# Kernel optimization log

Measured on AMD Instinct MI355X. Metric: run time of the kernel, lower is better.

Reference implementation:

```python
import jax, jax.numpy as jnp
import numpy as np
import math

B, L, D_MODEL = 8, 1024, 512
D_INNER = 1024          # expand*d_model
D2 = D_INNER // 2       # per-branch channels
DT_RANK = 32            # ceil(d_model/16)
D_STATE = 16
K = 4                   # d_conv
HIDDEN = 4 * D_MODEL


def setup_inputs() -> dict:
    key = jax.random.key(0)
    ks = jax.random.split(key, 12)
    rn = lambda k, s, sc: jax.random.normal(k, s, jnp.float32) * sc
    x = rn(ks[0], (B, L, D_MODEL), 1.0)
    in_proj_w = rn(ks[1], (D_INNER, D_MODEL), D_MODEL ** -0.5)
    conv_x_w = rn(ks[2], (D2, 1, K), 0.2)
    conv_z_w = rn(ks[3], (D2, 1, K), 0.2)
    x_proj_w = rn(ks[4], (DT_RANK + 2 * D_STATE, D2), D2 ** -0.5)
    dt_proj_w = rn(ks[5], (D2, DT_RANK), DT_RANK ** -0.5)
    dt = jnp.exp(jax.random.uniform(ks[6], (D2,)) * (math.log(0.1) - math.log(0.001)) + math.log(0.001))
    dt_proj_b = dt + jnp.log(-jnp.expm1(-dt))  # inverse softplus
    A_log = jnp.log(jnp.tile(jnp.arange(1, D_STATE + 1, dtype=jnp.float32)[None, :], (D2, 1)))
    ssm_D = jnp.ones((D2,), jnp.float32)
    out_proj_w = rn(ks[7], (D_MODEL, D_INNER), D_INNER ** -0.5)
    fc1_w = rn(ks[8], (HIDDEN, D_MODEL), D_MODEL ** -0.5)
    fc2_w = rn(ks[9], (D_MODEL, HIDDEN), HIDDEN ** -0.5)
    return dict(x=x,
                ln1_w=jnp.ones((D_MODEL,)), ln1_b=jnp.zeros((D_MODEL,)),
                in_proj_w=in_proj_w, conv_x_w=conv_x_w, conv_z_w=conv_z_w,
                x_proj_w=x_proj_w, dt_proj_w=dt_proj_w, dt_proj_b=dt_proj_b,
                A_log=A_log, ssm_D=ssm_D, out_proj_w=out_proj_w,
                ln2_w=jnp.ones((D_MODEL,)), ln2_b=jnp.zeros((D_MODEL,)),
                fc1_w=fc1_w, fc1_b=jnp.zeros((HIDDEN,)),
                fc2_w=fc2_w, fc2_b=jnp.zeros((D_MODEL,)))


def _layernorm(x, w, b, eps=1e-5):
    m = jnp.mean(x, -1, keepdims=True)
    v = jnp.mean((x - m) ** 2, -1, keepdims=True)
    return (x - m) * jax.lax.rsqrt(v + eps) * w + b


def _dwconv1d_same(x, w):
    # x: (b, c, l); w: (c, 1, K). torch 'same' for even K pads (left=1, right=2)
    return jax.lax.conv_general_dilated(
        x, w, window_strides=(1,), padding=[(1, 2)],
        dimension_numbers=('NCH', 'OIH', 'NCH'), feature_group_count=x.shape[1])


def _selective_scan(u, delta, A, Bc, Cc, Dp):
    # u, delta: (b, d, l); A: (d, n); Bc, Cc: (b, n, l); Dp: (d,)
    dA = jnp.exp(delta[..., None] * A[None, :, None, :])            # (b,d,l,n)
    Bt = jnp.moveaxis(Bc, 2, 1)                                     # (b,l,n)
    dBu = (delta * u)[..., None] * Bt[:, None, :, :]                # (b,d,l,n)
    dA_l = jnp.moveaxis(dA, 2, 0)                                   # (l,b,d,n)
    dBu_l = jnp.moveaxis(dBu, 2, 0)

    def step(h, t):
        dAt, dBut = t
        h = dAt * h + dBut
        return h, h

    h0 = jnp.zeros((u.shape[0], u.shape[1], A.shape[1]), u.dtype)
    _, hs = jax.lax.scan(step, h0, (dA_l, dBu_l))                   # hs: (l,b,d,n)
    Ct = jnp.moveaxis(Cc, 2, 0)                                     # (l,b,n)
    y = jnp.einsum('lbdn,lbn->bdl', hs, Ct)
    return y + Dp[None, :, None] * u


def _mixer(xn, in_proj_w, conv_x_w, conv_z_w, x_proj_w, dt_proj_w, dt_proj_b, A_log, ssm_D, out_proj_w):
    # xn: (b, l, d_model)
    xz = jnp.einsum('bld,ed->bel', xn, in_proj_w)                   # (b, d_inner, l)
    xh, zh = jnp.split(xz, 2, axis=1)                               # (b, d2, l) each
    xh = jax.nn.silu(_dwconv1d_same(xh, conv_x_w))
    zh = jax.nn.silu(_dwconv1d_same(zh, conv_z_w))
    x_dbl = jnp.einsum('bdl,rd->brl', xh, x_proj_w)                 # (b, R+2n, l)
    dt, Bc, Cc = jnp.split(x_dbl, [DT_RANK, DT_RANK + D_STATE], axis=1)
    dt = jnp.einsum('brl,dr->bdl', dt, dt_proj_w)
    delta = jax.nn.softplus(dt + dt_proj_b[None, :, None])          # delta_bias + delta_softplus
    A = -jnp.exp(A_log)
    y = _selective_scan(xh, delta, A, Bc, Cc, ssm_D)                # (b, d2, l)
    out = jnp.concatenate([y, zh], axis=1)                          # (b, d_inner, l)
    return jnp.einsum('bdl,ed->ble', out, out_proj_w)               # (b, l, d_model)


def reference(x, ln1_w, ln1_b, in_proj_w, conv_x_w, conv_z_w, x_proj_w, dt_proj_w, dt_proj_b,
              A_log, ssm_D, out_proj_w, ln2_w, ln2_b, fc1_w, fc1_b, fc2_w, fc2_b):
    h = x + _mixer(_layernorm(x, ln1_w, ln1_b), in_proj_w, conv_x_w, conv_z_w,
                   x_proj_w, dt_proj_w, dt_proj_b, A_log, ssm_D, out_proj_w)
    h2 = _layernorm(h, ln2_w, ln2_b)
    mlp = jax.nn.gelu(h2 @ fc1_w.T + fc1_b, approximate=False) @ fc2_w.T + fc2_b
    return h + mlp
```

## Files before the change

kernel.cpp:

```cpp
#include <hip/hip_runtime.h>
#include <stdint.h>


#define MROWS 8192
#define LSEQ 1024
#define DMODEL 512
#define DINNER 1024
#define D2 512
#define NSTATE 16
#define HIDDEN 2048
#define NCHUNK 32
#define LCHUNK 32

typedef unsigned short us;
typedef short short8 __attribute__((ext_vector_type(8)));
typedef float floatx4 __attribute__((ext_vector_type(4)));

__device__ __forceinline__ us f2bf(float f) {
    unsigned int u = __float_as_uint(f);
    u = (u + 0x7fffu + ((u >> 16) & 1u)) >> 16;
    return (us)u;
}
__device__ __forceinline__ float bf2f(us u) {
    return __uint_as_float(((unsigned int)u) << 16);
}

__device__ __forceinline__ void g2lds16(const void* g, void* l) {
    typedef __attribute__((address_space(1))) void GV;
    typedef __attribute__((address_space(3))) void LV;
    GV* gp = (GV*)(uintptr_t)g;
    LV* lp = (LV*)(uint32_t)(uintptr_t)l;
    __builtin_amdgcn_global_load_lds(gp, lp, 16, 0, 0);
}

__device__ __forceinline__ void pack_slot(const float* __restrict__ w,
                                          us* __restrict__ dst, int K, int sig)
{
    int lane = sig & 63;
    int KS = K >> 5;
    int ks = (sig >> 6) % KS;
    int g = sig / (KS << 6);
    const float* src = w + (size_t)(g * 16 + (lane & 15)) * K
                         + ks * 32 + (lane >> 4) * 8;
    short8 o;
    #pragma unroll
    for (int e = 0; e < 8; e++) o[e] = (short)f2bf(src[e]);
    *(short8*)(dst + (size_t)sig * 8) = o;
}

__global__ __launch_bounds__(256) void cvt_pack6(
    const float* __restrict__ w0, const float* __restrict__ w1,
    const float* __restrict__ w2, const float* __restrict__ w3,
    const float* __restrict__ w4, const float* __restrict__ w5,
    us* __restrict__ o0, us* __restrict__ o1, us* __restrict__ o2,
    us* __restrict__ o3, us* __restrict__ o4, us* __restrict__ o5)
{
    int bx = blockIdx.x, t = threadIdx.x;
    if (bx < 256)        pack_slot(w0, o0, 512,  bx * 256 + t);
    else if (bx < 272)   pack_slot(w1, o1, 512,  (bx - 256) * 256 + t);
    else if (bx < 280)   pack_slot(w2, o2, 32,   (bx - 272) * 256 + t);
    else if (bx < 536)   pack_slot(w3, o3, 1024, (bx - 280) * 256 + t);
    else if (bx < 1048)  pack_slot(w4, o4, 512,  (bx - 536) * 256 + t);
    else                 pack_slot(w5, o5, 2048, (bx - 1048) * 256 + t);
}

__global__ __launch_bounds__(256) void ln_pack(
    const float* __restrict__ x, const float* __restrict__ w,
    const float* __restrict__ b, us* __restrict__ outp)
{
    int g = blockIdx.x, t = threadIdx.x;
    __shared__ float T[16][516];
    __shared__ float mu[16], rs[16];
    const float* src = x + (size_t)g * 16 * DMODEL;
    #pragma unroll
    for (int p = 0; p < 8; p++) {
        int idx4 = p * 256 + t;
        int row = idx4 >> 7, c = (idx4 & 127) << 2;
        float4 v = *(const float4*)(src + (size_t)row * DMODEL + c);
        *(float4*)&T[row][c] = v;
    }
    __syncthreads();
    int r = t >> 4, i = t & 15;
    float s = 0.f, ss = 0.f;
    #pragma unroll
    for (int c = 0; c < 32; c++) {
        float v = T[r][c * 16 + i];
        s += v; ss += v * v;
    }
    #pragma unroll
    for (int off = 8; off > 0; off >>= 1) {
        s += __shfl_down(s, off, 16);
        ss += __shfl_down(ss, off, 16);
    }
    if (i == 0) {
        float m = s * (1.f / DMODEL);
        mu[r] = m;
        rs[r] = rsqrtf(ss * (1.f / DMODEL) - m * m + 1e-5f);
    }
    __syncthreads();
    #pragma unroll
    for (int s0 = 0; s0 < 4; s0++) {
        int sig = t * 4 + s0;
        int lane = sig & 63, ks = sig >> 6;
        int lr = lane & 15, lq = lane >> 4;
        int k0 = ks * 32 + lq * 8;
        float m = mu[lr], r2 = rs[lr];
        short8 o;
        #pragma unroll
        for (int e = 0; e < 8; e++)
            o[e] = (short)f2bf((T[lr][k0 + e] - m) * r2 * w[k0 + e] + b[k0 + e]);
        *(short8*)(outp + (size_t)g * 8192 + sig * 8) = o;
    }
}

#define MO_ROWBF16 0
#define MO_F32_PACK 1
#define MO_SOFTPLUS 2
#define MO_RES 3
#define MO_GELU_PACK 4
#define MO_BIAS_RES 5

template <int MODE, int BN>
__global__ __launch_bounds__(256) void gemm_pk2(
    const us* __restrict__ Ap, const us* __restrict__ Bp, int K,
    int Nout, int ldc,
    float* __restrict__ outF, us* __restrict__ outB, us* __restrict__ outP,
    const float* __restrict__ bias, const float* __restrict__ res)
{
    constexpr int NBg = BN / 16;
    constexpr int NJ = BN / 32;
    constexpr int TS = 8 + 2 * NBg;
    constexpr int PS = TS / 4;
    constexpr int STG = TS * 1024;
    constexpr int TTS = 32 * (BN + 4) * 4;
    constexpr int SM = STG > TTS ? STG : TTS;
    __shared__ __align__(16) char smraw[SM];
    us* sA = (us*)smraw;
    us* sB = sA + 8 * 512;
    float (*TT)[BN + 4] = (float (*)[BN + 4])smraw;

    int t = threadIdx.x;
    int lane = t & 63, w = t >> 6;
    int lr = lane & 15, lq = lane >> 4;
    int m0 = blockIdx.x * 64, n0 = blockIdx.y * BN;
    int gA0 = blockIdx.x * 4;
    int gB0 = blockIdx.y * NBg;
    int KS32 = K >> 5;

    floatx4 acc[2][NJ];
    #pragma unroll
    for (int i = 0; i < 2; i++)
        #pragma unroll
        for (int j = 0; j < NJ; j++) acc[i][j] = (floatx4){0.f, 0.f, 0.f, 0.f};

    for (int k64 = 0; k64 * 64 < K; k64++) {
        #pragma unroll
        for (int s = 0; s < PS; s++) {
            int slot = w * PS + s;
            if (slot < 8) {
                int g = slot >> 1, kl = slot & 1;
                g2lds16(Ap + ((size_t)(gA0 + g) * KS32 + k64 * 2 + kl) * 512
                           + lane * 8,
                        sA + slot * 512);
            } else {
                int sl = slot - 8;
                int j = sl >> 1, kl = sl & 1;
                g2lds16(Bp + ((size_t)(gB0 + j) * KS32 + k64 * 2 + kl) * 512
                           + lane * 8,
                        sB + sl * 512);
            }
        }
        __syncthreads();
        #pragma unroll
        for (int kl = 0; kl < 2; kl++) {
            short8 af[2], bfv[NJ];
            #pragma unroll
            for (int i = 0; i < 2; i++)
                af[i] = *(const short8*)(sA + (((w & 1) * 2 + i) * 2 + kl) * 512
                                         + lane * 8);
            #pragma unroll
            for (int j = 0; j < NJ; j++)
                bfv[j] = *(const short8*)(sB + (((w >> 1) * NJ + j) * 2 + kl) * 512
                                          + lane * 8);
            #pragma unroll
            for (int i = 0; i < 2; i++)
                #pragma unroll
                for (int j = 0; j < NJ; j++)
                    acc[i][j] = __builtin_amdgcn_mfma_f32_16x16x32_bf16(
                        af[i], bfv[j], acc[i][j], 0, 0, 0);
        }
        __syncthreads();
    }

    #pragma unroll
    for (int h = 0; h < 2; h++) {
        if ((w & 1) == h) {
            #pragma unroll
            for (int i = 0; i < 2; i++)
                #pragma unroll
                for (int j = 0; j < NJ; j++)
                    #pragma unroll
                    for (int r = 0; r < 4; r++)
                        TT[i * 16 + lq * 4 + r]
                          [(w >> 1) * (BN / 2) + j * 16 + lr] = acc[i][j][r];
        }
        __syncthreads();

        if (MODE == MO_ROWBF16) {
            constexpr int passes = 32 * BN / 8 / 256;
            #pragma unroll
            for (int p = 0; p < passes; p++) {
                int idx = p * 256 + t;
                int row = idx / (BN / 8);
                int c = (idx % (BN / 8)) * 8;
                short8 o8;
                #pragma unroll
                for (int e = 0; e < 8; e++) o8[e] = (short)f2bf(TT[row][c + e]);
                *(short8*)(outB + (size_t)(m0 + h * 32 + row) * ldc + n0 + c) = o8;
            }
        }
        if (MODE == MO_F32_PACK || MODE == MO_RES || MODE == MO_BIAS_RES) {
            constexpr int passes = 32 * BN / 4 / 256;
            #pragma unroll
            for (int p = 0; p < passes; p++) {
                int idx = p * 256 + t;
                int row = idx / (BN / 4);
                int c = (idx % (BN / 4)) * 4;
                float4 v = *(float4*)&TT[row][c];
                int col = n0 + c;
                size_t o = (size_t)(m0 + h * 32 + row) * ldc + col;
                float4 ov;
                if (MODE == MO_RES) {
                    float4 rv = *(const float4*)(res + o);
                    ov.x = v.x + rv.x; ov.y = v.y + rv.y;
                    ov.z = v.z + rv.z; ov.w = v.w + rv.w;
                } else if (MODE == MO_BIAS_RES) {
                    float4 rv = *(const float4*)(res + o);
                    float4 bv = *(const float4*)(bias + col);
                    ov.x = v.x + bv.x + rv.x; ov.y = v.y + bv.y + rv.y;
                    ov.z = v.z + bv.z + rv.z; ov.w = v.w + bv.w + rv.w;
                } else {
                    ov = v;
                }
                *(float4*)(outF + o) = ov;
            }
        }
        if (MODE == MO_F32_PACK || MODE == MO_GELU_PACK) {
            constexpr int passes = 4 * BN / 256;
            #pragma unroll
            for (int p = 0; p < passes; p++) {
                int sig = p * 256 + t;
                int gi = sig / (2 * BN);
                int rem = sig % (2 * BN);
                int ksl = rem >> 6;
                int ln2 = rem & 63;
                int lr2 = ln2 & 15, lq2 = ln2 >> 4;
                short8 o8;
                #pragma unroll
                for (int e = 0; e < 8; e++) {
                    float vv = TT[gi * 16 + lr2][ksl * 32 + lq2 * 8 + e];
                    if (MODE == MO_GELU_PACK) {
                        float tb = vv + bias[n0 + ksl * 32 + lq2 * 8 + e];
                        vv = 0.5f * tb * (1.f + erff(tb * 0.70710678118f));
                    }
                    o8[e] = (short)f2bf(vv);
                }
                *(short8*)(outP + ((size_t)((m0 >> 4) + h * 2 + gi) * Nout
                           + n0 + ksl * 32) * 16 + ln2 * 8) = o8;
            }
        }
        __syncthreads();
    }
}

template <int MODE, int BN>
__global__ __launch_bounds__(256) void gemm_pk(
    const us* __restrict__ Ap, int KA,
    const us* __restrict__ Bp, int KB, int Kloop,
    int Nout, int ldc,
    float* __restrict__ outF, us* __restrict__ outB, us* __restrict__ outP,
    const float* __restrict__ bias, const float* __restrict__ res)
{
    constexpr int NBg = BN / 16;
    constexpr int NJ = BN / 32;
    constexpr int TS = 4 + NBg;
    constexpr int PS = TS / 4;
    constexpr int SMSZ = 64 * (BN + 4) * 4;
    __shared__ __align__(16) char smraw[SMSZ];
    us* sA = (us*)smraw;
    us* sB = sA + 2048;
    float (*TT)[BN + 4] = (float (*)[BN + 4])smraw;

    int t = threadIdx.x;
    int lane = t & 63, w = t >> 6;
    int lr = lane & 15, lq = lane >> 4;
    int m0 = blockIdx.x * 64, n0 = blockIdx.y * BN;
    int gA0 = blockIdx.x * 4;
    int gB0 = n0 >> 4;

    floatx4 acc[2][NJ];
    #pragma unroll
    for (int i = 0; i < 2; i++)
        #pragma unroll
        for (int j = 0; j < NJ; j++) acc[i][j] = (floatx4){0.f, 0.f, 0.f, 0.f};

    for (int ks = 0; ks * 32 < Kloop; ks++) {
        #pragma unroll
        for (int s = 0; s < PS; s++) {
            int slot = w * PS + s;
            if (slot < 4)
                g2lds16(Ap + ((size_t)(gA0 + slot) * KA + ks * 32) * 16 + lane * 8,
                        sA + slot * 512);
            else
                g2lds16(Bp + ((size_t)(gB0 + slot - 4) * KB + ks * 32) * 16 + lane * 8,
                        sB + (slot - 4) * 512);
        }
        __syncthreads();
        short8 af[2], bfv[NJ];
        #pragma unroll
        for (int i = 0; i < 2; i++)
            af[i] = *(const short8*)(sA + ((w & 1) * 2 + i) * 512 + lane * 8);
        #pragma unroll
        for (int j = 0; j < NJ; j++)
            bfv[j] = *(const short8*)(sB + ((w >> 1) * NJ + j) * 512 + lane * 8);
        #pragma unroll
        for (int i = 0; i < 2; i++)
            #pragma unroll
            for (int j = 0; j < NJ; j++)
                acc[i][j] = __builtin_amdgcn_mfma_f32_16x16x32_bf16(
                    af[i], bfv[j], acc[i][j], 0, 0, 0);
        __syncthreads();
    }

    #pragma unroll
    for (int i = 0; i < 2; i++)
        #pragma unroll
        for (int j = 0; j < NJ; j++)
            #pragma unroll
            for (int r = 0; r < 4; r++)
                TT[(w & 1) * 32 + i * 16 + lq * 4 + r]
                  [(w >> 1) * (BN / 2) + j * 16 + lr] = acc[i][j][r];
    __syncthreads();

    if (MODE == MO_SOFTPLUS) {
        constexpr int passes = 64 * BN / 4 / 256;
        #pragma unroll
        for (int p = 0; p < passes; p++) {
            int idx = p * 256 + t;
            int row = idx / (BN / 4);
            int c = (idx % (BN / 4)) * 4;
            float4 v = *(float4*)&TT[row][c];
            int col = n0 + c;
            size_t o = (size_t)(m0 + row) * ldc + col;
            float vv[4] = {v.x, v.y, v.z, v.w};
            float oo[4];
            #pragma unroll
            for (int e = 0; e < 4; e++) {
                float tb = vv[e] + bias[col + e];
                oo[e] = (tb > 20.f) ? tb : log1pf(__expf(tb));
            }
            float4 ov = {oo[0], oo[1], oo[2], oo[3]};
            *(float4*)(outF + o) = ov;
        }
    }
}

__global__ __launch_bounds__(256) void conv_pk(
    const us* __restrict__ xz, const float* __restrict__ cwx,
    const float* __restrict__ cwz, float* __restrict__ xh_f,
    us* __restrict__ xh_p, us* __restrict__ outbuf_p)
{
    int bx = blockIdx.x, t = threadIdx.x;
    int b = bx >> 6, g = bx & 63;
    size_t rowbase = (size_t)b * LSEQ;
    #pragma unroll
    for (int s = 0; s < 4; s++) {
        int sig = t * 4 + s;
        int ks = sig >> 6, lane = sig & 63;
        int lr = lane & 15, lq = lane >> 4;
        int l = g * 16 + lr;
        int d0 = ks * 32 + lq * 8;
        float ax[8] = {0, 0, 0, 0, 0, 0, 0, 0};
        #pragma unroll
        for (int kk = 0; kk < 4; kk++) {
            int ls = l + kk - 1;
            if (ls >= 0 && ls < LSEQ) {
                const us* src = xz + (rowbase + ls) * DINNER + d0;
                #pragma unroll
                for (int e = 0; e < 8; e++)
                    ax[e] += cwx[(d0 + e) * 4 + kk] * bf2f(src[e]);
            }
        }
        short8 o8;
        float vo[8];
        #pragma unroll
        for (int e = 0; e < 8; e++) {
            float v = ax[e];
            v = v / (1.f + __expf(-v));
            vo[e] = v;
            o8[e] = (short)f2bf(v);
        }
        *(short8*)(xh_p + (size_t)bx * 8192 + sig * 8) = o8;
        float* fo = xh_f + (rowbase + l) * D2 + d0;
        float4 f0 = {vo[0], vo[1], vo[2], vo[3]};
        float4 f1 = {vo[4], vo[5], vo[6], vo[7]};
        *(float4*)fo = f0;
        *(float4*)(fo + 4) = f1;
    }
    #pragma unroll
    for (int s = 0; s < 4; s++) {
        int sig = t * 4 + s;
        int ks = sig >> 6, lane = sig & 63;
        int lr = lane & 15, lq = lane >> 4;
        int l = g * 16 + lr;
        int d0 = ks * 32 + lq * 8;
        float az[8] = {0, 0, 0, 0, 0, 0, 0, 0};
        #pragma unroll
        for (int kk = 0; kk < 4; kk++) {
            int ls = l + kk - 1;
            if (ls >= 0 && ls < LSEQ) {
                const us* src = xz + (rowbase + ls) * DINNER + 512 + d0;
                #pragma unroll
                for (int e = 0; e < 8; e++)
                    az[e] += cwz[(d0 + e) * 4 + kk] * bf2f(src[e]);
            }
        }
        short8 o8;
        #pragma unroll
        for (int e = 0; e < 8; e++) {
            float v = az[e];
            v = v / (1.f + __expf(-v));
            o8[e] = (short)f2bf(v);
        }
        *(short8*)(outbuf_p + (size_t)bx * 16384 + 8192 + sig * 8) = o8;
    }
}

__global__ __launch_bounds__(256) void scan_phase1(
    const float* __restrict__ delta, const float* __restrict__ u,
    const float* __restrict__ xdbl, const float* __restrict__ A_log,
    float* __restrict__ S, float* __restrict__ P)
{
    int bx = blockIdx.x;
    int b = bx >> 6, rem = bx & 63, c = rem >> 1, half = rem & 1;
    int d = half * 256 + threadIdx.x;
    float A2[NSTATE], h[NSTATE];
    #pragma unroll
    for (int n = 0; n < NSTATE; n++) {
        A2[n] = -__expf(A_log[d * NSTATE + n]) * 1.44269504f;
        h[n] = 0.f;
    }
    float sdt = 0.f;
    int l0 = c * LCHUNK;
    for (int l = l0; l < l0 + LCHUNK; ++l) {
        size_t idx = (size_t)(b * LSEQ + l);
        float dv = delta[idx * D2 + d];
        float uv = u[idx * D2 + d];
        float du = dv * uv;
        const float4* Bp = (const float4*)(xdbl + idx * 64 + 32);
        float4 B0 = Bp[0], B1 = Bp[1], B2 = Bp[2], B3 = Bp[3];
        float Bn[16] = {B0.x, B0.y, B0.z, B0.w, B1.x, B1.y, B1.z, B1.w,
                        B2.x, B2.y, B2.z, B2.w, B3.x, B3.y, B3.z, B3.w};
        sdt += dv;
        #pragma unroll
        for (int n = 0; n < NSTATE; n++)
            h[n] = exp2f(dv * A2[n]) * h[n] + du * Bn[n];
    }
    size_t o = ((size_t)(b * D2 + d)) * (NCHUNK * NSTATE) + c * NSTATE;
    #pragma unroll
    for (int n = 0; n < NSTATE; n++) {
        S[o + n] = h[n];
        P[o + n] = exp2f(sdt * A2[n]);
    }
}

__global__ __launch_bounds__(256) void scan_phase2(
    const float* __restrict__ S, const float* __restrict__ P,
    float* __restrict__ hin)
{
    int gid = blockIdx.x * 256 + threadIdx.x;
    int n = gid & 15;
    size_t base = ((size_t)(gid >> 4)) * (NCHUNK * NSTATE) + n;
    float h = 0.f;
    for (int c = 0; c < NCHUNK; c++) {
        size_t o = base + c * NSTATE;
        hin[o] = h;
        h = P[o] * h + S[o];
    }
}

__global__ __launch_bounds__(256) void scan_phase3(
    const float* __restrict__ delta, const float* __restrict__ u,
    const float* __restrict__ xdbl, const float* __restrict__ hin,
    const float* __restrict__ A_log, const float* __restrict__ Dvec,
    us* __restrict__ outbuf_p)
{
    int bx = blockIdx.x;
    int b = bx >> 6, rem = bx & 63, c = rem >> 1, half = rem & 1;
    int t = threadIdx.x;
    int d = half * 256 + t;
    __shared__ us yl[LCHUNK][264];
    float A2[NSTATE], h[NSTATE];
    size_t hb = ((size_t)(b * D2 + d)) * (NCHUNK * NSTATE) + c * NSTATE;
    #pragma unroll
    for (int n = 0; n < NSTATE; n++) {
        A2[n] = -__expf(A_log[d * NSTATE + n]) * 1.44269504f;
        h[n] = hin[hb + n];
    }
    float Dd = Dvec[d];
    int l0 = c * LCHUNK;
    for (int l = l0; l < l0 + LCHUNK; ++l) {
        size_t idx = (size_t)(b * LSEQ + l);
        float dv = delta[idx * D2 + d];
        float uv = u[idx * D2 + d];
        float du = dv * uv;
        const float4* Bp = (const float4*)(xdbl + idx * 64 + 32);
        const float4* Cp = (const float4*)(xdbl + idx * 64 + 48);
        float4 B0 = Bp[0], B1 = Bp[1], B2 = Bp[2], B3 = Bp[3];
        float4 C0 = Cp[0], C1 = Cp[1], C2 = Cp[2], C3 = Cp[3];
        float Bn[16] = {B0.x, B0.y, B0.z, B0.w, B1.x, B1.y, B1.z, B1.w,
                        B2.x, B2.y, B2.z, B2.w, B3.x, B3.y, B3.z, B3.w};
        float Cn[16] = {C0.x, C0.y, C0.z, C0.w, C1.x, C1.y, C1.z, C1.w,
                        C2.x, C2.y, C2.z, C2.w, C3.x, C3.y, C3.z, C3.w};
        float y = Dd * uv;
        #pragma unroll
        for (int n = 0; n < NSTATE; n++) {
            h[n] = exp2f(dv * A2[n]) * h[n] + du * Bn[n];
            y += h[n] * Cn[n];
        }
        yl[l - l0][t] = f2bf(y);
    }
    __syncthreads();
    int g0 = (b * LSEQ + l0) >> 4;
    #pragma unroll
    for (int s = 0; s < 4; s++) {
        int sig = t * 4 + s;
        int gi = sig >> 9;
        int rem2 = sig & 511;
        int ksl = rem2 >> 6;
        int lane = rem2 & 63;
        int lr = lane & 15, lq = lane >> 4;
        uint4 v = *(uint4*)&yl[gi * 16 + lr][ksl * 32 + lq * 8];
        *(uint4*)(outbuf_p + ((size_t)(g0 + gi) * 1024 + (half * 8 + ksl) * 32) * 16
                  + lane * 8) = v;
    }
}

extern "C" void kernel_launch(void* const* d_in, const int* in_sizes, int n_in,
                              void* d_out, int out_size, void* d_ws, size_t ws_size,
                              hipStream_t stream)
{
    const float* x         = (const float*)d_in[0];
    const float* ln1_w     = (const float*)d_in[1];
    const float* ln1_b     = (const float*)d_in[2];
    const float* in_proj_w = (const float*)d_in[3];
    const float* conv_x_w  = (const float*)d_in[4];
    const float* conv_z_w  = (const float*)d_in[5];
    const float* x_proj_w  = (const float*)d_in[6];
    const float* dt_proj_w = (const float*)d_in[7];
    const float* dt_proj_b = (const float*)d_in[8];
    const float* A_log     = (const float*)d_in[9];
    const float* ssm_D     = (const float*)d_in[10];
    const float* out_proj_w= (const float*)d_in[11];
    const float* ln2_w     = (const float*)d_in[12];
    const float* ln2_b     = (const float*)d_in[13];
    const float* fc1_w     = (const float*)d_in[14];
    const float* fc1_b     = (const float*)d_in[15];
    const float* fc2_w     = (const float*)d_in[16];
    const float* fc2_b     = (const float*)d_in[17];
    float* out = (float*)d_out;

    char* p = (char*)d_ws;
    us* wp_in  = (us*)(p);
    us* wp_x   = (us*)(p + 1048576);
    us* wp_dt  = (us*)(p + 1114112);
    us* wp_out = (us*)(p + 1146880);
    us* wp_f1  = (us*)(p + 2195456);
    us* wp_f2  = (us*)(p + 4292608);
    us*    xn_p    = (us*)(p + 6389760);
    us*    xz      = (us*)(p + 14778368);
    us*    xh_p    = (us*)(p + 31555584);
    float* xh_f    = (float*)(p + 39944192);
    us*    outbuf_p= (us*)(p + 56721408);
    float* xdbl_f  = (float*)(p + 73498624);
    us*    xdbl_p  = (us*)(p + 75595776);
    float* delta_f = (float*)(p + 76644352);
    float* h_f     = (float*)(p + 106004480);
    us*    h2_p    = xn_p;
    us*    mlp1_p  = xz;
    float* scanS = (float*)(p + 14778368);
    float* scanP = (float*)(p + 14778368 + 8388608);
    float* hin   = (float*)(p + 6389760);

    cvt_pack6<<<1560, 256, 0, stream>>>(in_proj_w, x_proj_w, dt_proj_w,
        out_proj_w, fc1_w, fc2_w, wp_in, wp_x, wp_dt, wp_out, wp_f1, wp_f2);

    ln_pack<<<512, 256, 0, stream>>>(x, ln1_w, ln1_b, xn_p);

    gemm_pk2<MO_ROWBF16, 128><<<dim3(128, 8), 256, 0, stream>>>(
        xn_p, wp_in, 512, 0, DINNER, nullptr, xz, nullptr, nullptr, nullptr);

    conv_pk<<<512, 256, 0, stream>>>(xz, conv_x_w, conv_z_w, xh_f, xh_p, outbuf_p);

    gemm_pk2<MO_F32_PACK, 64><<<dim3(128, 1), 256, 0, stream>>>(
        xh_p, wp_x, 512, 64, 64, xdbl_f, nullptr, xdbl_p, nullptr, nullptr);

    gemm_pk<MO_SOFTPLUS, 64><<<dim3(128, 8), 256, 0, stream>>>(
        xdbl_p, 64, wp_dt, 32, 32, 0, D2,
        delta_f, nullptr, nullptr, dt_proj_b, nullptr);

    scan_phase1<<<512, 256, 0, stream>>>(delta_f, xh_f, xdbl_f, A_log, scanS, scanP);
    scan_phase2<<<256, 256, 0, stream>>>(scanS, scanP, hin);
    scan_phase3<<<512, 256, 0, stream>>>(delta_f, xh_f, xdbl_f, hin, A_log,
        ssm_D, outbuf_p);

    gemm_pk2<MO_RES, 128><<<dim3(128, 4), 256, 0, stream>>>(
        outbuf_p, wp_out, 1024, 0, DMODEL, h_f, nullptr, nullptr, nullptr, x);

    ln_pack<<<512, 256, 0, stream>>>(h_f, ln2_w, ln2_b, h2_p);

    gemm_pk2<MO_GELU_PACK, 128><<<dim3(128, 16), 256, 0, stream>>>(
        h2_p, wp_f1, 512, HIDDEN, 0, nullptr, nullptr, mlp1_p, fc1_b, nullptr);

    gemm_pk2<MO_BIAS_RES, 128><<<dim3(128, 4), 256, 0, stream>>>(
        mlp1_p, wp_f2, 2048, 0, DMODEL, out, nullptr, nullptr, fc2_b, h_f);
}
```

Before: 328.7 us.

## Store delta and conv output in bf16, use tanh GELU, narrow output GEMM tiles

The softplus GEMM now writes delta as bf16, and the conv kernel writes its fp32 side-copy of xh as bf16. Both scan phases read these halved streams and convert back. The exact erf GELU is replaced with a tanh-form approximation built on exp. The out_proj and fc2 GEMMs switch from BN=128 to BN=64 with twice as many blocks for better occupancy. Together these cut memory traffic and special-function cost, at some numerical-accuracy risk in the scan and the MLP.

```diff
diff --git a/kernel.cpp b/kernel.cpp
--- a/kernel.cpp
+++ b/kernel.cpp
@@ -24,6 +24,11 @@
 __device__ __forceinline__ float bf2f(us u) {
     return __uint_as_float(((unsigned int)u) << 16);
 }
+__device__ __forceinline__ float gelu_fast(float x) {
+    float u = 1.59576912f * (x + 0.044715f * x * x * x);
+    float e = __expf(u);
+    return x * e / (e + 1.f);
+}
 
 __device__ __forceinline__ void g2lds16(const void* g, void* l) {
     typedef __attribute__((address_space(1))) void GV;
@@ -115,7 +120,7 @@
 
 #define MO_ROWBF16 0
 #define MO_F32_PACK 1
-#define MO_SOFTPLUS 2
+#define MO_SOFTPLUS_BF16 2
 #define MO_RES 3
 #define MO_GELU_PACK 4
 #define MO_BIAS_RES 5
@@ -261,7 +266,7 @@
                     float vv = TT[gi * 16 + lr2][ksl * 32 + lq2 * 8 + e];
                     if (MODE == MO_GELU_PACK) {
                         float tb = vv + bias[n0 + ksl * 32 + lq2 * 8 + e];
-                        vv = 0.5f * tb * (1.f + erff(tb * 0.70710678118f));
+                        vv = gelu_fast(tb);
                     }
                     o8[e] = (short)f2bf(vv);
                 }
@@ -342,32 +347,29 @@
                   [(w >> 1) * (BN / 2) + j * 16 + lr] = acc[i][j][r];
     __syncthreads();
 
-    if (MODE == MO_SOFTPLUS) {
-        constexpr int passes = 64 * BN / 4 / 256;
+    if (MODE == MO_SOFTPLUS_BF16) {
+        constexpr int passes = 64 * BN / 8 / 256;
         #pragma unroll
         for (int p = 0; p < passes; p++) {
             int idx = p * 256 + t;
-            int row = idx / (BN / 4);
-            int c = (idx % (BN / 4)) * 4;
-            float4 v = *(float4*)&TT[row][c];
+            int row = idx / (BN / 8);
+            int c = (idx % (BN / 8)) * 8;
             int col = n0 + c;
-            size_t o = (size_t)(m0 + row) * ldc + col;
-            float vv[4] = {v.x, v.y, v.z, v.w};
-            float oo[4];
-            #pragma unroll
-            for (int e = 0; e < 4; e++) {
-                float tb = vv[e] + bias[col + e];
-                oo[e] = (tb > 20.f) ? tb : log1pf(__expf(tb));
+            short8 o8;
+            #pragma unroll
+            for (int e = 0; e < 8; e++) {
+                float tb = TT[row][c + e] + bias[col + e];
+                float sp = (tb > 20.f) ? tb : log1pf(__expf(tb));
+                o8[e] = (short)f2bf(sp);
             }
-            float4 ov = {oo[0], oo[1], oo[2], oo[3]};
-            *(float4*)(outF + o) = ov;
+            *(short8*)(outB + (size_t)(m0 + row) * ldc + col) = o8;
         }
     }
 }
 
 __global__ __launch_bounds__(256) void conv_pk(
     const us* __restrict__ xz, const float* __restrict__ cwx,
-    const float* __restrict__ cwz, float* __restrict__ xh_f,
+    const float* __restrict__ cwz, us* __restrict__ xh_b,
     us* __restrict__ xh_p, us* __restrict__ outbuf_p)
 {
     int bx = blockIdx.x, t = threadIdx.x;
@@ -392,20 +394,14 @@
             }
         }
         short8 o8;
-        float vo[8];
         #pragma unroll
         for (int e = 0; e < 8; e++) {
             float v = ax[e];
             v = v / (1.f + __expf(-v));
-            vo[e] = v;
             o8[e] = (short)f2bf(v);
         }
         *(short8*)(xh_p + (size_t)bx * 8192 + sig * 8) = o8;
-        float* fo = xh_f + (rowbase + l) * D2 + d0;
-        float4 f0 = {vo[0], vo[1], vo[2], vo[3]};
-        float4 f1 = {vo[4], vo[5], vo[6], vo[7]};
-        *(float4*)fo = f0;
-        *(float4*)(fo + 4) = f1;
+        *(short8*)(xh_b + (rowbase + l) * D2 + d0) = o8;
     }
     #pragma unroll
     for (int s = 0; s < 4; s++) {
@@ -437,7 +433,7 @@
 }
 
 __global__ __launch_bounds__(256) void scan_phase1(
-    const float* __restrict__ delta, const float* __restrict__ u,
+    const us* __restrict__ delta, const us* __restrict__ u,
     const float* __restrict__ xdbl, const float* __restrict__ A_log,
     float* __restrict__ S, float* __restrict__ P)
 {
@@ -454,8 +450,8 @@
     int l0 = c * LCHUNK;
     for (int l = l0; l < l0 + LCHUNK; ++l) {
         size_t idx = (size_t)(b * LSEQ + l);
-        float dv = delta[idx * D2 + d];
-        float uv = u[idx * D2 + d];
+        float dv = bf2f(delta[idx * D2 + d]);
+        float uv = bf2f(u[idx * D2 + d]);
         float du = dv * uv;
         const float4* Bp = (const float4*)(xdbl + idx * 64 + 32);
         float4 B0 = Bp[0], B1 = Bp[1], B2 = Bp[2], B3 = Bp[3];
@@ -490,7 +486,7 @@
 }
 
 __global__ __launch_bounds__(256) void scan_phase3(
-    const float* __restrict__ delta, const float* __restrict__ u,
+    const us* __restrict__ delta, const us* __restrict__ u,
     const float* __restrict__ xdbl, const float* __restrict__ hin,
     const float* __restrict__ A_log, const float* __restrict__ Dvec,
     us* __restrict__ outbuf_p)
@@ -511,8 +507,8 @@
     int l0 = c * LCHUNK;
     for (int l = l0; l < l0 + LCHUNK; ++l) {
         size_t idx = (size_t)(b * LSEQ + l);
-        float dv = delta[idx * D2 + d];
-        float uv = u[idx * D2 + d];
+        float dv = bf2f(delta[idx * D2 + d]);
+        float uv = bf2f(u[idx * D2 + d]);
         float du = dv * uv;
         const float4* Bp = (const float4*)(xdbl + idx * 64 + 32);
         const float4* Cp = (const float4*)(xdbl + idx * 64 + 48);
@@ -580,11 +576,11 @@
     us*    xn_p    = (us*)(p + 6389760);
     us*    xz      = (us*)(p + 14778368);
     us*    xh_p    = (us*)(p + 31555584);
-    float* xh_f    = (float*)(p + 39944192);
+    us*    xh_b    = (us*)(p + 39944192);
     us*    outbuf_p= (us*)(p + 56721408);
     float* xdbl_f  = (float*)(p + 73498624);
     us*    xdbl_p  = (us*)(p + 75595776);
-    float* delta_f = (float*)(p + 76644352);
+    us*    delta_b = (us*)(p + 76644352);
     float* h_f     = (float*)(p + 106004480);
     us*    h2_p    = xn_p;
     us*    mlp1_p  = xz;
@@ -600,21 +596,21 @@
     gemm_pk2<MO_ROWBF16, 128><<<dim3(128, 8), 256, 0, stream>>>(
         xn_p, wp_in, 512, 0, DINNER, nullptr, xz, nullptr, nullptr, nullptr);
 
-    conv_pk<<<512, 256, 0, stream>>>(xz, conv_x_w, conv_z_w, xh_f, xh_p, outbuf_p);
+    conv_pk<<<512, 256, 0, stream>>>(xz, conv_x_w, conv_z_w, xh_b, xh_p, outbuf_p);
 
     gemm_pk2<MO_F32_PACK, 64><<<dim3(128, 1), 256, 0, stream>>>(
         xh_p, wp_x, 512, 64, 64, xdbl_f, nullptr, xdbl_p, nullptr, nullptr);
 
-    gemm_pk<MO_SOFTPLUS, 64><<<dim3(128, 8), 256, 0, stream>>>(
+    gemm_pk<MO_SOFTPLUS_BF16, 64><<<dim3(128, 8), 256, 0, stream>>>(
         xdbl_p, 64, wp_dt, 32, 32, 0, D2,
-        delta_f, nullptr, nullptr, dt_proj_b, nullptr);
-
-    scan_phase1<<<512, 256, 0, stream>>>(delta_f, xh_f, xdbl_f, A_log, scanS, scanP);
+        nullptr, delta_b, nullptr, dt_proj_b, nullptr);
+
+    scan_phase1<<<512, 256, 0, stream>>>(delta_b, xh_b, xdbl_f, A_log, scanS, scanP);
     scan_phase2<<<256, 256, 0, stream>>>(scanS, scanP, hin);
-    scan_phase3<<<512, 256, 0, stream>>>(delta_f, xh_f, xdbl_f, hin, A_log,
+    scan_phase3<<<512, 256, 0, stream>>>(delta_b, xh_b, xdbl_f, hin, A_log,
         ssm_D, outbuf_p);
 
-    gemm_pk2<MO_RES, 128><<<dim3(128, 4), 256, 0, stream>>>(
+    gemm_pk2<MO_RES, 64><<<dim3(128, 8), 256, 0, stream>>>(
         outbuf_p, wp_out, 1024, 0, DMODEL, h_f, nullptr, nullptr, nullptr, x);
 
     ln_pack<<<512, 256, 0, stream>>>(h_f, ln2_w, ln2_b, h2_p);
@@ -622,6 +618,6 @@
     gemm_pk2<MO_GELU_PACK, 128><<<dim3(128, 16), 256, 0, stream>>>(
         h2_p, wp_f1, 512, HIDDEN, 0, nullptr, nullptr, mlp1_p, fc1_b, nullptr);
 
-    gemm_pk2<MO_BIAS_RES, 128><<<dim3(128, 4), 256, 0, stream>>>(
+    gemm_pk2<MO_BIAS_RES, 64><<<dim3(128, 8), 256, 0, stream>>>(
         mlp1_p, wp_f2, 2048, 0, DMODEL, out, nullptr, nullptr, fc2_b, h_f);
 }
```

New measurement: 330.4 us. No clear change (+0.5%).
